# Kernel tuning notes

Measured on AMD Instinct MI355X. Metric: run time of the kernel, lower is better.

## Reference

```python
import jax, jax.numpy as jnp
import numpy as np

L_NOOBJ = 3.0


def _scale_loss(pred, gt, modulus, mask_pos, mask_neg):
    # pred/gt: [B,H,W,A,5+C]; modulus: [B,H,W,A,6]; mask_pos: [B,H,W,A] bool; mask_neg: same shape as pred, bool
    C = pred.shape[-1] - 5
    mpos = mask_pos.astype(pred.dtype)[..., None]           # broadcast over channel dim
    n_pos = jnp.sum(mask_pos)
    n_pos_f = jnp.maximum(n_pos, 1).astype(pred.dtype)
    # modulus weight of the LAST positive cell (reproduces box_param[ground_index][0] after the loop)
    flat = mask_pos.reshape(-1)
    idx_last = flat.shape[0] - 1 - jnp.argmax(flat[::-1])
    w_last = modulus.reshape(-1, 6)[idx_last, 0]
    diff2 = (gt - pred) ** 2 * mpos
    coord = w_last * jnp.sum(diff2[..., 0:4]) / n_pos_f
    conf_pos = jnp.sum(diff2[..., 4]) / n_pos_f
    # BCEWithLogitsLoss (mean over selected rows x C elements), numerically stable form
    x = pred[..., 5:]
    z = gt[..., 5:]
    bce = jnp.maximum(x, 0.0) - x * z + jnp.log1p(jnp.exp(-jnp.abs(x)))
    classify = jnp.sum(bce * mpos) / (n_pos_f * C)
    pos_loss = jnp.where(n_pos > 0, coord + conf_pos + classify, 0.0)
    # negative: elementwise masked MSE over full tensor, scaled by l_noobj
    mneg = mask_neg.astype(pred.dtype)
    n_neg = jnp.sum(mask_neg)
    neg = L_NOOBJ * jnp.sum(((gt - pred) ** 2) * mneg) / jnp.maximum(n_neg, 1).astype(pred.dtype)
    neg_loss = jnp.where(n_neg > 0, neg, 0.0)
    return pos_loss + neg_loss


def setup_inputs() -> dict:
    key = jax.random.key(0)
    B, A, C = 16, 3, 80
    sizes = {"small": 76, "middle": 38, "big": 19}
    out = {}
    k = key
    for name, g in sizes.items():
        k, k1, k2, k3, k4, k5 = jax.random.split(k, 6)
        out[f"{name}_pred"] = jax.random.normal(k1, (B, g, g, A, 5 + C), dtype=jnp.float32)
        out[f"{name}_gt"] = jax.random.uniform(k2, (B, g, g, A, 5 + C), dtype=jnp.float32)
        out[f"{name}_modulus"] = jax.random.uniform(k3, (B, g, g, A, 6), dtype=jnp.float32) + 0.5
        out[f"{name}_mask_pos"] = jax.random.bernoulli(k4, 0.01, (B, g, g, A))
        out[f"{name}_mask_neg"] = jax.random.bernoulli(k5, 0.3, (B, g, g, A, 5 + C))
    return out


def reference(small_pred, small_gt, small_modulus, small_mask_pos, small_mask_neg,
              middle_pred, middle_gt, middle_modulus, middle_mask_pos, middle_mask_neg,
              big_pred, big_gt, big_modulus, big_mask_pos, big_mask_neg):
    loss = (_scale_loss(small_pred, small_gt, small_modulus, small_mask_pos, small_mask_neg)
            + _scale_loss(middle_pred, middle_gt, middle_modulus, middle_mask_pos, middle_mask_neg)
            + _scale_loss(big_pred, big_gt, big_modulus, big_mask_pos, big_mask_neg))
    return loss
```

## Files before the change

kernel.cpp:

```cpp
#include <hip/hip_runtime.h>

typedef unsigned int u32;

#define NE0 23566080u
#define NE1 5891520u
#define NE2 1472880u
#define NBLK 2048u

struct ScaleAcc {
  float sum_coord, sum_conf, sum_bce, sum_neg;
  u32 n_pos, n_neg, max_idx, pad;
};

__device__ __forceinline__ void reduce_and_commit(
    float sc, float sf, float sb, float sn, u32 np, u32 nn, u32 mi,
    ScaleAcc* __restrict__ slot)
{
  #pragma unroll
  for (int o = 32; o > 0; o >>= 1) {
    sc += __shfl_down(sc, o);
    sf += __shfl_down(sf, o);
    sb += __shfl_down(sb, o);
    sn += __shfl_down(sn, o);
    np += __shfl_down(np, o);
    nn += __shfl_down(nn, o);
    u32 omi = __shfl_down(mi, o);
    mi = omi > mi ? omi : mi;
  }
  __shared__ float shf[4][4];
  __shared__ u32 shu[3][4];
  const int wave = threadIdx.x >> 6;
  const int lane = threadIdx.x & 63;
  if (lane == 0) {
    shf[0][wave] = sc; shf[1][wave] = sf; shf[2][wave] = sb; shf[3][wave] = sn;
    shu[0][wave] = np; shu[1][wave] = nn; shu[2][wave] = mi;
  }
  __syncthreads();
  if (threadIdx.x == 0) {
    ScaleAcc a = {0.f, 0.f, 0.f, 0.f, 0u, 0u, 0u, 0u};
    #pragma unroll
    for (int w = 0; w < 4; ++w) {
      a.sum_coord += shf[0][w]; a.sum_conf += shf[1][w];
      a.sum_bce   += shf[2][w]; a.sum_neg  += shf[3][w];
      a.n_pos += shu[0][w]; a.n_neg += shu[1][w];
      a.max_idx = shu[2][w] > a.max_idx ? shu[2][w] : a.max_idx;
    }
    *slot = a;
  }
  __syncthreads();
}

__device__ __forceinline__ void process_scale(
    const float* __restrict__ pred, const float* __restrict__ gt,
    const int* __restrict__ mpos, const int* __restrict__ mneg,
    u32 ngroups, u32 tid, u32 nthreads, ScaleAcc* __restrict__ slot)
{
  float sc = 0.f, sf = 0.f, sb = 0.f, sn = 0.f;
  u32 np = 0, nn = 0, mi = 0;
  const float4* p4 = (const float4*)pred;
  const float4* g4 = (const float4*)gt;
  const int4*   m4 = (const int4*)mneg;
  for (u32 g = tid; g < ngroups; g += nthreads) {
    float4 pv = p4[g];
    float4 gv = g4[g];
    int4   mv = m4[g];
    u32 base = g * 4u;
    u32 cell = base / 85u;
    u32 ch = base - cell * 85u;
    float ps[4] = {pv.x, pv.y, pv.z, pv.w};
    float gs[4] = {gv.x, gv.y, gv.z, gv.w};
    int   ms[4] = {mv.x, mv.y, mv.z, mv.w};
    #pragma unroll
    for (int j = 0; j < 4; ++j) {
      float x = ps[j], z = gs[j];
      float d = z - x;
      float d2 = d * d;
      if (ms[j]) { sn += d2; nn++; }
      if (mpos[cell]) {
        if (ch == 0u) { np++; mi = cell > mi ? cell : mi; }
        if (ch < 4u)        sc += d2;
        else if (ch == 4u)  sf += d2;
        else                sb += fmaxf(x, 0.f) - x * z + log1pf(__expf(-fabsf(x)));
      }
      ++ch;
      if (ch == 85u) { ch = 0u; ++cell; }
    }
  }
  reduce_and_commit(sc, sf, sb, sn, np, nn, mi, slot);
}

__global__ __launch_bounds__(256) void yolo_main(
    const float* __restrict__ pred0, const float* __restrict__ gt0,
    const int* __restrict__ mp0, const int* __restrict__ mn0,
    const float* __restrict__ pred1, const float* __restrict__ gt1,
    const int* __restrict__ mp1, const int* __restrict__ mn1,
    const float* __restrict__ pred2, const float* __restrict__ gt2,
    const int* __restrict__ mp2, const int* __restrict__ mn2,
    ScaleAcc* __restrict__ ws)
{
  const u32 tid = blockIdx.x * blockDim.x + threadIdx.x;
  const u32 nthreads = gridDim.x * blockDim.x;
  process_scale(pred0, gt0, mp0, mn0, NE0 / 4u, tid, nthreads, &ws[0 * NBLK + blockIdx.x]);
  process_scale(pred1, gt1, mp1, mn1, NE1 / 4u, tid, nthreads, &ws[1 * NBLK + blockIdx.x]);
  process_scale(pred2, gt2, mp2, mn2, NE2 / 4u, tid, nthreads, &ws[2 * NBLK + blockIdx.x]);
}

__global__ __launch_bounds__(256) void yolo_reduce(
    const ScaleAcc* __restrict__ ws,
    const float* __restrict__ mod0, const float* __restrict__ mod1,
    const float* __restrict__ mod2, float* __restrict__ out)
{
  const float* mods[3] = {mod0, mod1, mod2};
  __shared__ float shf[4][4];
  __shared__ u32 shu[3][4];
  const int wave = threadIdx.x >> 6;
  const int lane = threadIdx.x & 63;
  float loss = 0.f;
  for (int s = 0; s < 3; ++s) {
    float sc = 0.f, sf = 0.f, sb = 0.f, sn = 0.f;
    u32 np = 0, nn = 0, mi = 0;
    for (u32 t = threadIdx.x; t < NBLK; t += 256u) {
      ScaleAcc a = ws[(u32)s * NBLK + t];
      sc += a.sum_coord; sf += a.sum_conf; sb += a.sum_bce; sn += a.sum_neg;
      np += a.n_pos; nn += a.n_neg;
      mi = a.max_idx > mi ? a.max_idx : mi;
    }
    #pragma unroll
    for (int o = 32; o > 0; o >>= 1) {
      sc += __shfl_down(sc, o);
      sf += __shfl_down(sf, o);
      sb += __shfl_down(sb, o);
      sn += __shfl_down(sn, o);
      np += __shfl_down(np, o);
      nn += __shfl_down(nn, o);
      u32 omi = __shfl_down(mi, o);
      mi = omi > mi ? omi : mi;
    }
    if (lane == 0) {
      shf[0][wave] = sc; shf[1][wave] = sf; shf[2][wave] = sb; shf[3][wave] = sn;
      shu[0][wave] = np; shu[1][wave] = nn; shu[2][wave] = mi;
    }
    __syncthreads();
    if (threadIdx.x == 0) {
      float a = 0.f, b = 0.f, c = 0.f, d = 0.f;
      u32 x = 0, y = 0, z = 0;
      #pragma unroll
      for (int w = 0; w < 4; ++w) {
        a += shf[0][w]; b += shf[1][w]; c += shf[2][w]; d += shf[3][w];
        x += shu[0][w]; y += shu[1][w];
        z = shu[2][w] > z ? shu[2][w] : z;
      }
      if (x > 0u) {
        float npf = (float)x;
        float w_last = mods[s][z * 6u];
        loss += (w_last * a + b + c * (1.f / 80.f)) / npf;
      }
      if (y > 0u) {
        loss += 3.0f * d / (float)y;
      }
    }
    __syncthreads();
  }
  if (threadIdx.x == 0) out[0] = loss;
}

extern "C" void kernel_launch(void* const* d_in, const int* in_sizes, int n_in,
                              void* d_out, int out_size, void* d_ws, size_t ws_size,
                              hipStream_t stream)
{
  const float* pred0 = (const float*)d_in[0];
  const float* gt0   = (const float*)d_in[1];
  const float* mod0  = (const float*)d_in[2];
  const int*   mp0   = (const int*)d_in[3];
  const int*   mn0   = (const int*)d_in[4];
  const float* pred1 = (const float*)d_in[5];
  const float* gt1   = (const float*)d_in[6];
  const float* mod1  = (const float*)d_in[7];
  const int*   mp1   = (const int*)d_in[8];
  const int*   mn1   = (const int*)d_in[9];
  const float* pred2 = (const float*)d_in[10];
  const float* gt2   = (const float*)d_in[11];
  const float* mod2  = (const float*)d_in[12];
  const int*   mp2   = (const int*)d_in[13];
  const int*   mn2   = (const int*)d_in[14];

  ScaleAcc* ws = (ScaleAcc*)d_ws;

  yolo_main<<<NBLK, 256, 0, stream>>>(pred0, gt0, mp0, mn0,
                                      pred1, gt1, mp1, mn1,
                                      pred2, gt2, mp2, mn2, ws);
  yolo_reduce<<<1, 256, 0, stream>>>(ws, mod0, mod1, mod2, (float*)d_out);
}
```

Measured before the change: 81.01 us.

## Split negative and positive loss into separate kernels with sparse per-cell positive pass

The single streaming kernel is replaced by a branchless negative-MSE streaming kernel that only reads pred, gt and mask_neg with two-way unrolled float4 loads. A second kernel handles positive cells, one thread per cell, and reads pred/gt rows only where mask_pos is set. This removes the per-element division by 85, the mpos lookup and the divergent BCE branch from the hot streaming loop. In exchange there is an extra launch, the positive pass makes scattered uncoalesced row reads, and the final reduce now combines two workspace arrays.

```diff
diff --git a/kernel.cpp b/kernel.cpp
--- a/kernel.cpp
+++ b/kernel.cpp
@@ -2,162 +2,206 @@
 
 typedef unsigned int u32;
 
-#define NE0 23566080u
-#define NE1 5891520u
-#define NE2 1472880u
+#define NG0 5891520u
+#define NG1 1472880u
+#define NG2 368220u
+#define NC0 277248u
+#define NC1 69312u
+#define NC2 17328u
 #define NBLK 2048u
-
-struct ScaleAcc {
-  float sum_coord, sum_conf, sum_bce, sum_neg;
-  u32 n_pos, n_neg, max_idx, pad;
-};
-
-__device__ __forceinline__ void reduce_and_commit(
-    float sc, float sf, float sb, float sn, u32 np, u32 nn, u32 mi,
-    ScaleAcc* __restrict__ slot)
-{
+#define PB0 1083u
+#define PB1 271u
+#define PB2 68u
+#define PBTOT (PB0 + PB1 + PB2)
+
+struct NegAcc { float sn; u32 nn; };
+struct PosAcc { float sc, sf, sb; u32 np, mi, pad[3]; };
+
+
+__device__ __forceinline__ void neg_body(const float4 pv, const float4 gv,
+                                         const int4 mv, float& sn, u32& nn)
+{
+  float d;
+  d = gv.x - pv.x; sn = fmaf(d * d, (float)mv.x, sn); nn += (u32)mv.x;
+  d = gv.y - pv.y; sn = fmaf(d * d, (float)mv.y, sn); nn += (u32)mv.y;
+  d = gv.z - pv.z; sn = fmaf(d * d, (float)mv.z, sn); nn += (u32)mv.z;
+  d = gv.w - pv.w; sn = fmaf(d * d, (float)mv.w, sn); nn += (u32)mv.w;
+}
+
+__device__ __forceinline__ void neg_scale(
+    const float* __restrict__ pred, const float* __restrict__ gt,
+    const int* __restrict__ mneg, u32 n, u32 tid, u32 stride,
+    NegAcc* __restrict__ slot)
+{
+  const float4* __restrict__ p4 = (const float4*)pred;
+  const float4* __restrict__ g4 = (const float4*)gt;
+  const int4*   __restrict__ m4 = (const int4*)mneg;
+  float sn = 0.f; u32 nn = 0;
+  const u32 iters = n / stride;
+  u32 i = 0;
+  for (; i + 2 <= iters; i += 2) {
+    u32 ga = tid + i * stride;
+    u32 gb = ga + stride;
+    float4 pa = p4[ga]; float4 qa = g4[ga]; int4 ma = m4[ga];
+    float4 pb = p4[gb]; float4 qb = g4[gb]; int4 mb = m4[gb];
+    neg_body(pa, qa, ma, sn, nn);
+    neg_body(pb, qb, mb, sn, nn);
+  }
+  if (i < iters) {
+    u32 ga = tid + i * stride;
+    neg_body(p4[ga], g4[ga], m4[ga], sn, nn);
+  }
+  u32 gl = tid + iters * stride;
+  if (gl < n) {
+    neg_body(p4[gl], g4[gl], m4[gl], sn, nn);
+  }
+  #pragma unroll
+  for (int o = 32; o > 0; o >>= 1) {
+    sn += __shfl_down(sn, o);
+    nn += __shfl_down((int)nn, o);
+  }
+  __shared__ float shf[4];
+  __shared__ u32 shu[4];
+  const int wave = threadIdx.x >> 6, lane = threadIdx.x & 63;
+  if (lane == 0) { shf[wave] = sn; shu[wave] = nn; }
+  __syncthreads();
+  if (threadIdx.x == 0) {
+    NegAcc a;
+    a.sn = shf[0] + shf[1] + shf[2] + shf[3];
+    a.nn = shu[0] + shu[1] + shu[2] + shu[3];
+    *slot = a;
+  }
+  __syncthreads();
+}
+
+__global__ __launch_bounds__(256) void yolo_neg(
+    const float* __restrict__ pred0, const float* __restrict__ gt0, const int* __restrict__ mn0,
+    const float* __restrict__ pred1, const float* __restrict__ gt1, const int* __restrict__ mn1,
+    const float* __restrict__ pred2, const float* __restrict__ gt2, const int* __restrict__ mn2,
+    NegAcc* __restrict__ neg)
+{
+  const u32 tid = blockIdx.x * blockDim.x + threadIdx.x;
+  const u32 stride = gridDim.x * blockDim.x;
+  neg_scale(pred0, gt0, mn0, NG0, tid, stride, &neg[0 * NBLK + blockIdx.x]);
+  neg_scale(pred1, gt1, mn1, NG1, tid, stride, &neg[1 * NBLK + blockIdx.x]);
+  neg_scale(pred2, gt2, mn2, NG2, tid, stride, &neg[2 * NBLK + blockIdx.x]);
+}
+
+
+__global__ __launch_bounds__(256) void yolo_pos(
+    const float* __restrict__ pred0, const float* __restrict__ gt0, const int* __restrict__ mp0,
+    const float* __restrict__ pred1, const float* __restrict__ gt1, const int* __restrict__ mp1,
+    const float* __restrict__ pred2, const float* __restrict__ gt2, const int* __restrict__ mp2,
+    PosAcc* __restrict__ pos)
+{
+  const u32 b = blockIdx.x;
+  const float* pred; const float* gtp; const int* mp; u32 nc, cell0;
+  if (b < PB0)            { pred = pred0; gtp = gt0; mp = mp0; nc = NC0; cell0 = b * 256u; }
+  else if (b < PB0 + PB1) { pred = pred1; gtp = gt1; mp = mp1; nc = NC1; cell0 = (b - PB0) * 256u; }
+  else                    { pred = pred2; gtp = gt2; mp = mp2; nc = NC2; cell0 = (b - PB0 - PB1) * 256u; }
+
+  const u32 cell = cell0 + threadIdx.x;
+  float sc = 0.f, sf = 0.f, sb = 0.f; u32 np = 0, mi = 0;
+  if (cell < nc && mp[cell] != 0) {
+    np = 1; mi = cell;
+    const float* __restrict__ pp = pred + (size_t)cell * 85u;
+    const float* __restrict__ gg = gtp  + (size_t)cell * 85u;
+    #pragma unroll
+    for (int ch = 0; ch < 4; ++ch) {
+      float x = pp[ch], z = gg[ch], d = z - x;
+      sc += d * d;
+    }
+    { float x = pp[4], z = gg[4], d = z - x; sf = d * d; }
+    #pragma unroll 16
+    for (int ch = 5; ch < 85; ++ch) {
+      float x = pp[ch], z = gg[ch];
+      sb += fmaxf(x, 0.f) - x * z + log1pf(__expf(-fabsf(x)));
+    }
+  }
   #pragma unroll
   for (int o = 32; o > 0; o >>= 1) {
     sc += __shfl_down(sc, o);
     sf += __shfl_down(sf, o);
     sb += __shfl_down(sb, o);
-    sn += __shfl_down(sn, o);
-    np += __shfl_down(np, o);
-    nn += __shfl_down(nn, o);
-    u32 omi = __shfl_down(mi, o);
-    mi = omi > mi ? omi : mi;
-  }
+    np += __shfl_down((int)np, o);
+    u32 om = __shfl_down((int)mi, o);
+    mi = om > mi ? om : mi;
+  }
+  __shared__ float shf[3][4];
+  __shared__ u32 shu[2][4];
+  const int wave = threadIdx.x >> 6, lane = threadIdx.x & 63;
+  if (lane == 0) {
+    shf[0][wave] = sc; shf[1][wave] = sf; shf[2][wave] = sb;
+    shu[0][wave] = np; shu[1][wave] = mi;
+  }
+  __syncthreads();
+  if (threadIdx.x == 0) {
+    PosAcc a = {0.f, 0.f, 0.f, 0u, 0u, {0u, 0u, 0u}};
+    #pragma unroll
+    for (int w = 0; w < 4; ++w) {
+      a.sc += shf[0][w]; a.sf += shf[1][w]; a.sb += shf[2][w];
+      a.np += shu[0][w];
+      a.mi = shu[1][w] > a.mi ? shu[1][w] : a.mi;
+    }
+    pos[b] = a;
+  }
+}
+
+
+__global__ __launch_bounds__(256) void yolo_final(
+    const NegAcc* __restrict__ neg, const PosAcc* __restrict__ pos,
+    const float* __restrict__ mod0, const float* __restrict__ mod1,
+    const float* __restrict__ mod2, float* __restrict__ out)
+{
+  const float* mods[3] = {mod0, mod1, mod2};
+  const u32 pbase[3] = {0u, PB0, PB0 + PB1};
+  const u32 pcnt[3]  = {PB0, PB1, PB2};
   __shared__ float shf[4][4];
   __shared__ u32 shu[3][4];
-  const int wave = threadIdx.x >> 6;
-  const int lane = threadIdx.x & 63;
-  if (lane == 0) {
-    shf[0][wave] = sc; shf[1][wave] = sf; shf[2][wave] = sb; shf[3][wave] = sn;
-    shu[0][wave] = np; shu[1][wave] = nn; shu[2][wave] = mi;
-  }
-  __syncthreads();
-  if (threadIdx.x == 0) {
-    ScaleAcc a = {0.f, 0.f, 0.f, 0.f, 0u, 0u, 0u, 0u};
-    #pragma unroll
-    for (int w = 0; w < 4; ++w) {
-      a.sum_coord += shf[0][w]; a.sum_conf += shf[1][w];
-      a.sum_bce   += shf[2][w]; a.sum_neg  += shf[3][w];
-      a.n_pos += shu[0][w]; a.n_neg += shu[1][w];
-      a.max_idx = shu[2][w] > a.max_idx ? shu[2][w] : a.max_idx;
-    }
-    *slot = a;
-  }
-  __syncthreads();
-}
-
-__device__ __forceinline__ void process_scale(
-    const float* __restrict__ pred, const float* __restrict__ gt,
-    const int* __restrict__ mpos, const int* __restrict__ mneg,
-    u32 ngroups, u32 tid, u32 nthreads, ScaleAcc* __restrict__ slot)
-{
-  float sc = 0.f, sf = 0.f, sb = 0.f, sn = 0.f;
-  u32 np = 0, nn = 0, mi = 0;
-  const float4* p4 = (const float4*)pred;
-  const float4* g4 = (const float4*)gt;
-  const int4*   m4 = (const int4*)mneg;
-  for (u32 g = tid; g < ngroups; g += nthreads) {
-    float4 pv = p4[g];
-    float4 gv = g4[g];
-    int4   mv = m4[g];
-    u32 base = g * 4u;
-    u32 cell = base / 85u;
-    u32 ch = base - cell * 85u;
-    float ps[4] = {pv.x, pv.y, pv.z, pv.w};
-    float gs[4] = {gv.x, gv.y, gv.z, gv.w};
-    int   ms[4] = {mv.x, mv.y, mv.z, mv.w};
-    #pragma unroll
-    for (int j = 0; j < 4; ++j) {
-      float x = ps[j], z = gs[j];
-      float d = z - x;
-      float d2 = d * d;
-      if (ms[j]) { sn += d2; nn++; }
-      if (mpos[cell]) {
-        if (ch == 0u) { np++; mi = cell > mi ? cell : mi; }
-        if (ch < 4u)        sc += d2;
-        else if (ch == 4u)  sf += d2;
-        else                sb += fmaxf(x, 0.f) - x * z + log1pf(__expf(-fabsf(x)));
-      }
-      ++ch;
-      if (ch == 85u) { ch = 0u; ++cell; }
-    }
-  }
-  reduce_and_commit(sc, sf, sb, sn, np, nn, mi, slot);
-}
-
-__global__ __launch_bounds__(256) void yolo_main(
-    const float* __restrict__ pred0, const float* __restrict__ gt0,
-    const int* __restrict__ mp0, const int* __restrict__ mn0,
-    const float* __restrict__ pred1, const float* __restrict__ gt1,
-    const int* __restrict__ mp1, const int* __restrict__ mn1,
-    const float* __restrict__ pred2, const float* __restrict__ gt2,
-    const int* __restrict__ mp2, const int* __restrict__ mn2,
-    ScaleAcc* __restrict__ ws)
-{
-  const u32 tid = blockIdx.x * blockDim.x + threadIdx.x;
-  const u32 nthreads = gridDim.x * blockDim.x;
-  process_scale(pred0, gt0, mp0, mn0, NE0 / 4u, tid, nthreads, &ws[0 * NBLK + blockIdx.x]);
-  process_scale(pred1, gt1, mp1, mn1, NE1 / 4u, tid, nthreads, &ws[1 * NBLK + blockIdx.x]);
-  process_scale(pred2, gt2, mp2, mn2, NE2 / 4u, tid, nthreads, &ws[2 * NBLK + blockIdx.x]);
-}
-
-__global__ __launch_bounds__(256) void yolo_reduce(
-    const ScaleAcc* __restrict__ ws,
-    const float* __restrict__ mod0, const float* __restrict__ mod1,
-    const float* __restrict__ mod2, float* __restrict__ out)
-{
-  const float* mods[3] = {mod0, mod1, mod2};
-  __shared__ float shf[4][4];
-  __shared__ u32 shu[3][4];
-  const int wave = threadIdx.x >> 6;
-  const int lane = threadIdx.x & 63;
+  const int wave = threadIdx.x >> 6, lane = threadIdx.x & 63;
   float loss = 0.f;
   for (int s = 0; s < 3; ++s) {
-    float sc = 0.f, sf = 0.f, sb = 0.f, sn = 0.f;
-    u32 np = 0, nn = 0, mi = 0;
+    float sn = 0.f, sc = 0.f, sf = 0.f, sb = 0.f;
+    u32 nn = 0, np = 0, mi = 0;
     for (u32 t = threadIdx.x; t < NBLK; t += 256u) {
-      ScaleAcc a = ws[(u32)s * NBLK + t];
-      sc += a.sum_coord; sf += a.sum_conf; sb += a.sum_bce; sn += a.sum_neg;
-      np += a.n_pos; nn += a.n_neg;
-      mi = a.max_idx > mi ? a.max_idx : mi;
+      NegAcc a = neg[(u32)s * NBLK + t];
+      sn += a.sn; nn += a.nn;
+    }
+    for (u32 t = threadIdx.x; t < pcnt[s]; t += 256u) {
+      PosAcc a = pos[pbase[s] + t];
+      sc += a.sc; sf += a.sf; sb += a.sb; np += a.np;
+      mi = a.mi > mi ? a.mi : mi;
     }
     #pragma unroll
     for (int o = 32; o > 0; o >>= 1) {
+      sn += __shfl_down(sn, o);
       sc += __shfl_down(sc, o);
       sf += __shfl_down(sf, o);
       sb += __shfl_down(sb, o);
-      sn += __shfl_down(sn, o);
-      np += __shfl_down(np, o);
-      nn += __shfl_down(nn, o);
-      u32 omi = __shfl_down(mi, o);
-      mi = omi > mi ? omi : mi;
+      nn += __shfl_down((int)nn, o);
+      np += __shfl_down((int)np, o);
+      u32 om = __shfl_down((int)mi, o);
+      mi = om > mi ? om : mi;
     }
     if (lane == 0) {
-      shf[0][wave] = sc; shf[1][wave] = sf; shf[2][wave] = sb; shf[3][wave] = sn;
-      shu[0][wave] = np; shu[1][wave] = nn; shu[2][wave] = mi;
+      shf[0][wave] = sn; shf[1][wave] = sc; shf[2][wave] = sf; shf[3][wave] = sb;
+      shu[0][wave] = nn; shu[1][wave] = np; shu[2][wave] = mi;
     }
     __syncthreads();
     if (threadIdx.x == 0) {
-      float a = 0.f, b = 0.f, c = 0.f, d = 0.f;
-      u32 x = 0, y = 0, z = 0;
+      float Sn = 0.f, Sc = 0.f, Sf = 0.f, Sb = 0.f;
+      u32 Nn = 0, Np = 0, Mi = 0;
       #pragma unroll
       for (int w = 0; w < 4; ++w) {
-        a += shf[0][w]; b += shf[1][w]; c += shf[2][w]; d += shf[3][w];
-        x += shu[0][w]; y += shu[1][w];
-        z = shu[2][w] > z ? shu[2][w] : z;
+        Sn += shf[0][w]; Sc += shf[1][w]; Sf += shf[2][w]; Sb += shf[3][w];
+        Nn += shu[0][w]; Np += shu[1][w];
+        Mi = shu[2][w] > Mi ? shu[2][w] : Mi;
       }
-      if (x > 0u) {
-        float npf = (float)x;
-        float w_last = mods[s][z * 6u];
-        loss += (w_last * a + b + c * (1.f / 80.f)) / npf;
+      if (Np > 0u) {
+        float w_last = mods[s][(size_t)Mi * 6u];
+        loss += (w_last * Sc + Sf + Sb * (1.f / 80.f)) / (float)Np;
       }
-      if (y > 0u) {
-        loss += 3.0f * d / (float)y;
-      }
+      if (Nn > 0u) loss += 3.0f * Sn / (float)Nn;
     }
     __syncthreads();
   }
@@ -184,10 +228,14 @@
   const int*   mp2   = (const int*)d_in[13];
   const int*   mn2   = (const int*)d_in[14];
 
-  ScaleAcc* ws = (ScaleAcc*)d_ws;
-
-  yolo_main<<<NBLK, 256, 0, stream>>>(pred0, gt0, mp0, mn0,
-                                      pred1, gt1, mp1, mn1,
-                                      pred2, gt2, mp2, mn2, ws);
-  yolo_reduce<<<1, 256, 0, stream>>>(ws, mod0, mod1, mod2, (float*)d_out);
-}
+  NegAcc* neg = (NegAcc*)d_ws;
+  PosAcc* pos = (PosAcc*)((char*)d_ws + 3 * NBLK * sizeof(NegAcc));
+
+  yolo_neg<<<NBLK, 256, 0, stream>>>(pred0, gt0, mn0,
+                                     pred1, gt1, mn1,
+                                     pred2, gt2, mn2, neg);
+  yolo_pos<<<PBTOT, 256, 0, stream>>>(pred0, gt0, mp0,
+                                      pred1, gt1, mp1,
+                                      pred2, gt2, mp2, pos);
+  yolo_final<<<1, 256, 0, stream>>>(neg, pos, mod0, mod1, mod2, (float*)d_out);
+}
```

Result: slower. 217.0 us (+167.9%).
